# Kernel optimization log

Hardware: AMD Instinct MI355X
Metric: run time of the kernel (lower is better)

Reference implementation:

```python
import jax, jax.numpy as jnp
import numpy as np

B = 4096   # batch_size from init_kwargs
D = 128    # embedding dim
TEMP = 0.25


def _l2_normalize(x, eps=1e-12):
    # matches F.normalize(dim=1): x / max(||x||, eps)
    n = jnp.linalg.norm(x, axis=1, keepdims=True)
    return x / jnp.maximum(n, eps)


def setup_inputs() -> dict:
    key = jax.random.key(0)
    k1, k2 = jax.random.split(key)
    return {
        "emb_i": jax.random.normal(k1, (B, D), dtype=jnp.float32),
        "emb_j": jax.random.normal(k2, (B, D), dtype=jnp.float32),
    }


def reference(emb_i, emb_j):
    b = emb_i.shape[0]
    z_i = _l2_normalize(emb_i)
    z_j = _l2_normalize(emb_j)
    reps = jnp.concatenate([z_i, z_j], axis=0)            # [2B, D]
    # cosine similarity of normalized vectors == dot product
    sim = reps @ reps.T                                    # [2B, 2B]
    sim_ij = jnp.diagonal(sim, offset=b)                   # [B]
    sim_ji = jnp.diagonal(sim, offset=-b)                  # [B]
    positives = jnp.concatenate([sim_ij, sim_ji], axis=0)  # [2B]
    # negatives_mask as overwritten in __init__: ones only on the two
    # off-diagonal cross-view blocks.
    mask = (
        jnp.zeros((2 * b, 2 * b), dtype=sim.dtype)
        .at[:b, b:].set(1.0)
        .at[b:, :b].set(1.0)
    )
    exp_sim = jnp.exp(sim / TEMP)                          # [2B, 2B]
    denom = jnp.sum(mask * exp_sim, axis=1)                # [2B]
    loss_partial = -jnp.log(jnp.exp(positives / TEMP) / denom)
    loss = jnp.sum(loss_partial) / (2 * b)
    return loss
```

## Files before the change

### kernel.cpp

```cpp
#include <hip/hip_runtime.h>
#include <hip/hip_bf16.h>

#define BATCH 4096
#define DIM   128
#define NT    32
#define EXP_SCALE 5.770780163555854f

typedef __bf16 bf16_t;
typedef __bf16 bf16x8 __attribute__((ext_vector_type(8)));
typedef float  f32x4  __attribute__((ext_vector_type(4)));

__global__ __launch_bounds__(256) void normalize_kernel(
    const float* __restrict__ emb_i, const float* __restrict__ emb_j,
    bf16_t* __restrict__ zi, bf16_t* __restrict__ zj, float* __restrict__ pos,
    float* __restrict__ denoms )
{
    if (blockIdx.x < 16) {
        int idx = (blockIdx.x * 256 + threadIdx.x) * 4;
        *(float4*)&denoms[idx] = make_float4(0.f, 0.f, 0.f, 0.f);
    }

    int wave = threadIdx.x >> 6;
    int lane = threadIdx.x & 63;
    int k = blockIdx.x * 4 + wave;

    const float2* ei = (const float2*)(emb_i + (size_t)k * DIM);
    const float2* ej = (const float2*)(emb_j + (size_t)k * DIM);
    float2 a = ei[lane];
    float2 b = ej[lane];

    float sii = a.x * a.x + a.y * a.y;
    float sjj = b.x * b.x + b.y * b.y;
    float sij = a.x * b.x + a.y * b.y;
#pragma unroll
    for (int m = 1; m < 64; m <<= 1) {
        sii += __shfl_xor(sii, m);
        sjj += __shfl_xor(sjj, m);
        sij += __shfl_xor(sij, m);
    }
    float inv_i = 1.0f / fmaxf(sqrtf(sii), 1e-12f);
    float inv_j = 1.0f / fmaxf(sqrtf(sjj), 1e-12f);

    struct bf16_2 { bf16_t x, y; };
    bf16_2 pi, pj;
    pi.x = (bf16_t)(a.x * inv_i);  pi.y = (bf16_t)(a.y * inv_i);
    pj.x = (bf16_t)(b.x * inv_j);  pj.y = (bf16_t)(b.y * inv_j);
    ((bf16_2*)(zi + (size_t)k * DIM))[lane] = pi;
    ((bf16_2*)(zj + (size_t)k * DIM))[lane] = pj;

    if (lane == 0) pos[k] = sij * inv_i * inv_j;
}

__global__ __launch_bounds__(256) void gemm_exp_kernel(
    const bf16_t* __restrict__ zi, const bf16_t* __restrict__ zj,
    float* __restrict__ rowDenom, float* __restrict__ colDenom)
{
    __shared__ __align__(16) bf16_t zi_s[128][136];
    __shared__ __align__(16) bf16_t zj_s[128][136];
    __shared__ float colRed[4][128];

    const int tid = threadIdx.x;
    const int ti = blockIdx.x, tj = blockIdx.y;

#pragma unroll
    for (int it = 0; it < 8; ++it) {
        int c = it * 256 + tid;
        int row = c >> 4;
        int col = (c & 15) << 3;
        *(uint4*)&zi_s[row][col] =
            *(const uint4*)(zi + ((size_t)(ti * 128 + row)) * DIM + col);
        *(uint4*)&zj_s[row][col] =
            *(const uint4*)(zj + ((size_t)(tj * 128 + row)) * DIM + col);
    }
    __syncthreads();

    const int wave = tid >> 6;
    const int lane = tid & 63;
    const int l15  = lane & 15;
    const int quad = lane >> 4;

    const f32x4 vzero = {0.f, 0.f, 0.f, 0.f};
    f32x4 acc[2][8];
#pragma unroll
    for (int rt = 0; rt < 2; ++rt)
#pragma unroll
        for (int ct = 0; ct < 8; ++ct) acc[rt][ct] = vzero;

#pragma unroll
    for (int ks = 0; ks < 4; ++ks) {
        int k0 = ks * 32 + quad * 8;
        bf16x8 afrag[2], bfrag[8];
#pragma unroll
        for (int rt = 0; rt < 2; ++rt)
            afrag[rt] = *(const bf16x8*)&zi_s[(wave * 2 + rt) * 16 + l15][k0];
#pragma unroll
        for (int ct = 0; ct < 8; ++ct)
            bfrag[ct] = *(const bf16x8*)&zj_s[ct * 16 + l15][k0];
#pragma unroll
        for (int rt = 0; rt < 2; ++rt)
#pragma unroll
            for (int ct = 0; ct < 8; ++ct)
                acc[rt][ct] = __builtin_amdgcn_mfma_f32_16x16x32_bf16(
                    afrag[rt], bfrag[ct], acc[rt][ct], 0, 0, 0);
    }

    float rowPart[2][4] = {{0.f, 0.f, 0.f, 0.f}, {0.f, 0.f, 0.f, 0.f}};
    float colPart[8]    = {0.f, 0.f, 0.f, 0.f, 0.f, 0.f, 0.f, 0.f};
#pragma unroll
    for (int rt = 0; rt < 2; ++rt)
#pragma unroll
        for (int ct = 0; ct < 8; ++ct)
#pragma unroll
            for (int r = 0; r < 4; ++r) {
                float e = exp2f(acc[rt][ct][r] * EXP_SCALE);
                rowPart[rt][r] += e;
                colPart[ct]    += e;
            }

#pragma unroll
    for (int rt = 0; rt < 2; ++rt)
#pragma unroll
        for (int r = 0; r < 4; ++r) {
            float v = rowPart[rt][r];
            v += __shfl_xor(v, 1);
            v += __shfl_xor(v, 2);
            v += __shfl_xor(v, 4);
            v += __shfl_xor(v, 8);
            if (l15 == 0) {
                int grow = ti * 128 + (wave * 2 + rt) * 16 + quad * 4 + r;
                atomicAdd(&rowDenom[grow], v);
            }
        }

#pragma unroll
    for (int ct = 0; ct < 8; ++ct) {
        float v = colPart[ct];
        v += __shfl_xor(v, 16);
        v += __shfl_xor(v, 32);
        if (quad == 0) colRed[wave][ct * 16 + l15] = v;
    }
    __syncthreads();
    if (tid < 128) {
        float s = colRed[0][tid] + colRed[1][tid] + colRed[2][tid] + colRed[3][tid];
        atomicAdd(&colDenom[tj * 128 + tid], s);
    }
}

__global__ __launch_bounds__(256) void finalize_kernel(
    const float* __restrict__ denoms, const float* __restrict__ pos,
    float* __restrict__ out)
{
    const float* rowDenom = denoms;
    const float* colDenom = denoms + BATCH;
    int tid = threadIdx.x;
    float acc = 0.f;
#pragma unroll
    for (int it = 0; it < 16; ++it) {
        int k = it * 256 + tid;
        acc += logf(rowDenom[k]) + logf(colDenom[k]) - 8.0f * pos[k];
    }
#pragma unroll
    for (int m = 1; m < 64; m <<= 1) acc += __shfl_xor(acc, m);
    __shared__ float red[4];
    if ((tid & 63) == 0) red[tid >> 6] = acc;
    __syncthreads();
    if (tid == 0)
        out[0] = (red[0] + red[1] + red[2] + red[3]) * (1.0f / (2.0f * BATCH));
}

extern "C" void kernel_launch(void* const* d_in, const int* in_sizes, int n_in,
                              void* d_out, int out_size, void* d_ws, size_t ws_size,
                              hipStream_t stream) {
    const float* emb_i = (const float*)d_in[0];
    const float* emb_j = (const float*)d_in[1];
    float* out = (float*)d_out;

    char* ws = (char*)d_ws;
    bf16_t* zi     = (bf16_t*)(ws);
    bf16_t* zj     = (bf16_t*)(ws + (1u << 20));
    float*  denoms = (float*)(ws + (2u << 20));
    float*  pos    = denoms + 2 * BATCH;

    normalize_kernel<<<BATCH / 4, 256, 0, stream>>>(emb_i, emb_j, zi, zj, pos, denoms);
    gemm_exp_kernel<<<dim3(NT, NT), 256, 0, stream>>>(zi, zj, denoms, denoms + BATCH);
    finalize_kernel<<<1, 256, 0, stream>>>(denoms, pos, out);
}
```

Measured before the change: 74.60 us.

## Fuse finalize into GEMM via last-block counter; widen normalize and load A fragments directly

Removes the separate finalize kernel launch: each GEMM block bumps a global counter, and the last block to finish computes the log-sum loss from the atomically accumulated denominators. The normalize kernel now has 16 threads per row with float4 loads and 16-byte bf16 stores, and it also resets the counter. The GEMM kernel loads its A-operand fragments straight from global memory into registers instead of staging them in shared memory, which halves LDS use. The trade-off is a threadfence plus atomic per block, and a serial tail reduction inside the last block.

```diff
diff --git a/kernel.cpp b/kernel.cpp
--- a/kernel.cpp
+++ b/kernel.cpp
@@ -4,6 +4,7 @@
 #define BATCH 4096
 #define DIM   128
 #define NT    32
+#define NBLK  (NT * NT)
 #define EXP_SCALE 5.770780163555854f
 
 typedef __bf16 bf16_t;
@@ -13,27 +14,32 @@
 __global__ __launch_bounds__(256) void normalize_kernel(
     const float* __restrict__ emb_i, const float* __restrict__ emb_j,
     bf16_t* __restrict__ zi, bf16_t* __restrict__ zj, float* __restrict__ pos,
-    float* __restrict__ denoms )
+    float* __restrict__ denoms , unsigned int* __restrict__ counter)
 {
-    if (blockIdx.x < 16) {
-        int idx = (blockIdx.x * 256 + threadIdx.x) * 4;
+    const int tid = threadIdx.x;
+    if (blockIdx.x < 8) {
+        int idx = (blockIdx.x * 256 + tid) * 4;
         *(float4*)&denoms[idx] = make_float4(0.f, 0.f, 0.f, 0.f);
     }
-
-    int wave = threadIdx.x >> 6;
-    int lane = threadIdx.x & 63;
-    int k = blockIdx.x * 4 + wave;
-
-    const float2* ei = (const float2*)(emb_i + (size_t)k * DIM);
-    const float2* ej = (const float2*)(emb_j + (size_t)k * DIM);
-    float2 a = ei[lane];
-    float2 b = ej[lane];
-
-    float sii = a.x * a.x + a.y * a.y;
-    float sjj = b.x * b.x + b.y * b.y;
-    float sij = a.x * b.x + a.y * b.y;
-#pragma unroll
-    for (int m = 1; m < 64; m <<= 1) {
+    if (blockIdx.x == 8 && tid == 0) *counter = 0u;
+
+    const int g  = tid >> 4;
+    const int gl = tid & 15;
+    const int k  = blockIdx.x * 16 + g;
+
+    const float4* pi4 = (const float4*)(emb_i + (size_t)k * DIM);
+    const float4* pj4 = (const float4*)(emb_j + (size_t)k * DIM);
+    float4 a0 = pi4[gl * 2], a1 = pi4[gl * 2 + 1];
+    float4 b0 = pj4[gl * 2], b1 = pj4[gl * 2 + 1];
+
+    float sii = a0.x*a0.x + a0.y*a0.y + a0.z*a0.z + a0.w*a0.w
+              + a1.x*a1.x + a1.y*a1.y + a1.z*a1.z + a1.w*a1.w;
+    float sjj = b0.x*b0.x + b0.y*b0.y + b0.z*b0.z + b0.w*b0.w
+              + b1.x*b1.x + b1.y*b1.y + b1.z*b1.z + b1.w*b1.w;
+    float sij = a0.x*b0.x + a0.y*b0.y + a0.z*b0.z + a0.w*b0.w
+              + a1.x*b1.x + a1.y*b1.y + a1.z*b1.z + a1.w*b1.w;
+#pragma unroll
+    for (int m = 1; m < 16; m <<= 1) {
         sii += __shfl_xor(sii, m);
         sjj += __shfl_xor(sjj, m);
         sij += __shfl_xor(sij, m);
@@ -41,44 +47,61 @@
     float inv_i = 1.0f / fmaxf(sqrtf(sii), 1e-12f);
     float inv_j = 1.0f / fmaxf(sqrtf(sjj), 1e-12f);
 
-    struct bf16_2 { bf16_t x, y; };
-    bf16_2 pi, pj;
-    pi.x = (bf16_t)(a.x * inv_i);  pi.y = (bf16_t)(a.y * inv_i);
-    pj.x = (bf16_t)(b.x * inv_j);  pj.y = (bf16_t)(b.y * inv_j);
-    ((bf16_2*)(zi + (size_t)k * DIM))[lane] = pi;
-    ((bf16_2*)(zj + (size_t)k * DIM))[lane] = pj;
-
-    if (lane == 0) pos[k] = sij * inv_i * inv_j;
+    bf16x8 oi, oj;
+    oi[0] = (bf16_t)(a0.x*inv_i); oi[1] = (bf16_t)(a0.y*inv_i);
+    oi[2] = (bf16_t)(a0.z*inv_i); oi[3] = (bf16_t)(a0.w*inv_i);
+    oi[4] = (bf16_t)(a1.x*inv_i); oi[5] = (bf16_t)(a1.y*inv_i);
+    oi[6] = (bf16_t)(a1.z*inv_i); oi[7] = (bf16_t)(a1.w*inv_i);
+    oj[0] = (bf16_t)(b0.x*inv_j); oj[1] = (bf16_t)(b0.y*inv_j);
+    oj[2] = (bf16_t)(b0.z*inv_j); oj[3] = (bf16_t)(b0.w*inv_j);
+    oj[4] = (bf16_t)(b1.x*inv_j); oj[5] = (bf16_t)(b1.y*inv_j);
+    oj[6] = (bf16_t)(b1.z*inv_j); oj[7] = (bf16_t)(b1.w*inv_j);
+    *(bf16x8*)(zi + (size_t)k * DIM + gl * 8) = oi;
+    *(bf16x8*)(zj + (size_t)k * DIM + gl * 8) = oj;
+
+    if (gl == 0) pos[k] = sij * inv_i * inv_j;
 }
 
 __global__ __launch_bounds__(256) void gemm_exp_kernel(
     const bf16_t* __restrict__ zi, const bf16_t* __restrict__ zj,
-    float* __restrict__ rowDenom, float* __restrict__ colDenom)
+    float* __restrict__ denoms, const float* __restrict__ pos,
+    unsigned int* __restrict__ counter, float* __restrict__ out)
 {
-    __shared__ __align__(16) bf16_t zi_s[128][136];
     __shared__ __align__(16) bf16_t zj_s[128][136];
     __shared__ float colRed[4][128];
+    __shared__ bool isLast;
+
+    float* rowDenom = denoms;
+    float* colDenom = denoms + BATCH;
 
     const int tid = threadIdx.x;
     const int ti = blockIdx.x, tj = blockIdx.y;
+    const int wave = tid >> 6;
+    const int lane = tid & 63;
+    const int l15  = lane & 15;
+    const int quad = lane >> 4;
+
+    bf16x8 afrag[2][4];
+    {
+        const bf16_t* base = zi + (size_t)(ti * 128) * DIM;
+#pragma unroll
+        for (int rt = 0; rt < 2; ++rt)
+#pragma unroll
+            for (int ks = 0; ks < 4; ++ks)
+                afrag[rt][ks] = *(const bf16x8*)(
+                    base + (size_t)((wave * 2 + rt) * 16 + l15) * DIM + ks * 32 + quad * 8);
+    }
 
 #pragma unroll
     for (int it = 0; it < 8; ++it) {
         int c = it * 256 + tid;
         int row = c >> 4;
         int col = (c & 15) << 3;
-        *(uint4*)&zi_s[row][col] =
-            *(const uint4*)(zi + ((size_t)(ti * 128 + row)) * DIM + col);
         *(uint4*)&zj_s[row][col] =
             *(const uint4*)(zj + ((size_t)(tj * 128 + row)) * DIM + col);
     }
     __syncthreads();
 
-    const int wave = tid >> 6;
-    const int lane = tid & 63;
-    const int l15  = lane & 15;
-    const int quad = lane >> 4;
-
     const f32x4 vzero = {0.f, 0.f, 0.f, 0.f};
     f32x4 acc[2][8];
 #pragma unroll
@@ -89,10 +112,7 @@
 #pragma unroll
     for (int ks = 0; ks < 4; ++ks) {
         int k0 = ks * 32 + quad * 8;
-        bf16x8 afrag[2], bfrag[8];
-#pragma unroll
-        for (int rt = 0; rt < 2; ++rt)
-            afrag[rt] = *(const bf16x8*)&zi_s[(wave * 2 + rt) * 16 + l15][k0];
+        bf16x8 bfrag[8];
 #pragma unroll
         for (int ct = 0; ct < 8; ++ct)
             bfrag[ct] = *(const bf16x8*)&zj_s[ct * 16 + l15][k0];
@@ -101,7 +121,7 @@
 #pragma unroll
             for (int ct = 0; ct < 8; ++ct)
                 acc[rt][ct] = __builtin_amdgcn_mfma_f32_16x16x32_bf16(
-                    afrag[rt], bfrag[ct], acc[rt][ct], 0, 0, 0);
+                    afrag[rt][ks], bfrag[ct], acc[rt][ct], 0, 0, 0);
     }
 
     float rowPart[2][4] = {{0.f, 0.f, 0.f, 0.f}, {0.f, 0.f, 0.f, 0.f}};
@@ -144,28 +164,33 @@
         float s = colRed[0][tid] + colRed[1][tid] + colRed[2][tid] + colRed[3][tid];
         atomicAdd(&colDenom[tj * 128 + tid], s);
     }
-}
-
-__global__ __launch_bounds__(256) void finalize_kernel(
-    const float* __restrict__ denoms, const float* __restrict__ pos,
-    float* __restrict__ out)
-{
-    const float* rowDenom = denoms;
-    const float* colDenom = denoms + BATCH;
-    int tid = threadIdx.x;
-    float acc = 0.f;
+
+    __threadfence();
+    __syncthreads();
+    if (tid == 0) {
+        unsigned int old = atomicAdd(counter, 1u);
+        isLast = (old == NBLK - 1);
+    }
+    __syncthreads();
+    if (!isLast) return;
+
+    float accv = 0.f;
 #pragma unroll
     for (int it = 0; it < 16; ++it) {
         int k = it * 256 + tid;
-        acc += logf(rowDenom[k]) + logf(colDenom[k]) - 8.0f * pos[k];
-    }
-#pragma unroll
-    for (int m = 1; m < 64; m <<= 1) acc += __shfl_xor(acc, m);
-    __shared__ float red[4];
-    if ((tid & 63) == 0) red[tid >> 6] = acc;
+        float r = __hip_atomic_load(&rowDenom[k], __ATOMIC_RELAXED,
+                                    __HIP_MEMORY_SCOPE_AGENT);
+        float c = __hip_atomic_load(&colDenom[k], __ATOMIC_RELAXED,
+                                    __HIP_MEMORY_SCOPE_AGENT);
+        accv += logf(r) + logf(c) - 8.0f * pos[k];
+    }
+#pragma unroll
+    for (int m = 1; m < 64; m <<= 1) accv += __shfl_xor(accv, m);
+    if (lane == 0) colRed[0][wave] = accv;
     __syncthreads();
     if (tid == 0)
-        out[0] = (red[0] + red[1] + red[2] + red[3]) * (1.0f / (2.0f * BATCH));
+        out[0] = (colRed[0][0] + colRed[0][1] + colRed[0][2] + colRed[0][3])
+                 * (1.0f / (2.0f * BATCH));
 }
 
 extern "C" void kernel_launch(void* const* d_in, const int* in_sizes, int n_in,
@@ -180,8 +205,10 @@
     bf16_t* zj     = (bf16_t*)(ws + (1u << 20));
     float*  denoms = (float*)(ws + (2u << 20));
     float*  pos    = denoms + 2 * BATCH;
-
-    normalize_kernel<<<BATCH / 4, 256, 0, stream>>>(emb_i, emb_j, zi, zj, pos, denoms);
-    gemm_exp_kernel<<<dim3(NT, NT), 256, 0, stream>>>(zi, zj, denoms, denoms + BATCH);
-    finalize_kernel<<<1, 256, 0, stream>>>(denoms, pos, out);
+    unsigned int* counter = (unsigned int*)(pos + BATCH);
+
+    normalize_kernel<<<BATCH / 16, 256, 0, stream>>>(emb_i, emb_j, zi, zj, pos,
+                                                     denoms, counter);
+    gemm_exp_kernel<<<dim3(NT, NT), 256, 0, stream>>>(zi, zj, denoms, pos,
+                                                      counter, out);
 }
```

Measured after the change: 133.8 us. 1.79x slower.
